# Optimization experiments

Hardware: AMD Instinct MI355X
Metric: run time of the kernel (lower is better)

## Reference

```python
import jax, jax.numpy as jnp
import numpy as np

D_MODEL = 2048
NUM_HEADS = 16
D_K = D_MODEL // NUM_HEADS  # 128, per-head dim used for RoPE
ROPE_THETA = 10000.0
MAX_SEQ_LEN = 2048
BATCH = 4
SEQ = 2048


def _trunc_normal(key, shape, std):
    # approximate trunc_normal_(mean=0, std, a=-3std, b=3std)
    return jnp.clip(std * jax.random.normal(key, shape), -3 * std, 3 * std)


def setup_inputs() -> dict:
    key = jax.random.key(0)
    ks = jax.random.split(key, 6)
    x = jax.random.normal(ks[0], (BATCH, SEQ, D_MODEL), dtype=jnp.float32)
    token_positions = jnp.arange(SEQ, dtype=jnp.int32)
    std = float(np.sqrt(2.0 / (D_MODEL + D_MODEL)))
    wq = _trunc_normal(ks[1], (D_MODEL, D_MODEL), std)  # (d_out, d_in)
    wk = _trunc_normal(ks[2], (D_MODEL, D_MODEL), std)
    wv = _trunc_normal(ks[3], (D_MODEL, D_MODEL), std)
    wo = _trunc_normal(ks[4], (D_MODEL, D_MODEL), std)
    return {"x": x, "token_positions": token_positions,
            "wq": wq, "wk": wk, "wv": wv, "wo": wo}


def _rope(t, pos):
    # t: (b, h, n, d_k), pos: (n,) int
    # interleaved pairs: (x1, x2) = (t[..., 0::2], t[..., 1::2])
    freqs = 1.0 / (ROPE_THETA ** (jnp.arange(0, D_K, 2, dtype=jnp.float32) / D_K))
    angles = pos.astype(jnp.float32)[:, None] * freqs[None, :]  # (n, d_k/2)
    cos = jnp.cos(angles).astype(t.dtype)
    sin = jnp.sin(angles).astype(t.dtype)
    tr = t.reshape(*t.shape[:-1], D_K // 2, 2)
    x1, x2 = tr[..., 0], tr[..., 1]
    y1 = cos * x1 - sin * x2
    y2 = sin * x1 + cos * x2
    return jnp.stack([y1, y2], axis=-1).reshape(t.shape)


def reference(x, token_positions, wq, wk, wv, wo):
    b, n, d = x.shape
    q = jnp.einsum('bnd,od->bno', x, wq)
    k = jnp.einsum('bnd,od->bno', x, wk)
    v = jnp.einsum('bnd,od->bno', x, wv)
    # split heads for RoPE: (b, n, h*dk) -> (b, h, n, dk)
    split = lambda t: t.reshape(b, n, NUM_HEADS, D_K).transpose(0, 2, 1, 3)
    merge = lambda t: t.transpose(0, 2, 1, 3).reshape(b, n, d)
    q = merge(_rope(split(q), token_positions))
    k = merge(_rope(split(k), token_positions))
    # NOTE: source merges heads back BEFORE flash attention -> single-head
    # attention over full d_model with causal mask, scale 1/sqrt(d_model)
    scale = 1.0 / jnp.sqrt(jnp.asarray(d, dtype=x.dtype))
    scores = jnp.einsum('bqd,bkd->bqk', q, k) * scale  # (b, n, n)
    causal = jnp.tril(jnp.ones((n, n), dtype=bool))
    scores = jnp.where(causal[None, :, :], scores, jnp.finfo(scores.dtype).min)
    attn = jax.nn.softmax(scores, axis=-1)
    out = jnp.einsum('bqk,bkd->bqd', attn, v)
    return jnp.einsum('bnd,od->bno', out, wo)
```

## Files before the change

### kernel.cpp

```cpp
#include <hip/hip_runtime.h>
#include <hip/hip_bf16.h>
#include <cstdint>
#include <cmath>

typedef __attribute__((ext_vector_type(4))) float f32x4;
typedef __attribute__((ext_vector_type(8))) short bf16x8;

#define BAR()   __builtin_amdgcn_s_barrier()
#define PRIO1() __builtin_amdgcn_s_setprio(1)
#define PRIO0() __builtin_amdgcn_s_setprio(0)
#define WAITV4() asm volatile("s_waitcnt vmcnt(4)" ::: "memory")
#define WAITV3() asm volatile("s_waitcnt vmcnt(3)" ::: "memory")
#define WAITV0() asm volatile("s_waitcnt vmcnt(0)" ::: "memory")
#define MM(a,b,c) __builtin_amdgcn_mfma_f32_16x16x32_bf16((a),(b),(c),0,0,0)

__device__ __forceinline__ void gl_lds16(const __hip_bfloat16* g, char* l) {
    __builtin_amdgcn_global_load_lds(
        (const __attribute__((address_space(1))) void*)g,
        (__attribute__((address_space(3))) void*)l, 16, 0, 0);
}
__device__ __forceinline__ void store_c(float* C, size_t i, float v) { C[i] = v; }
__device__ __forceinline__ void store_c(__hip_bfloat16* C, size_t i, float v) { C[i] = __float2bfloat16(v); }

#define STAGEA(nb, kt) do{ gl_lds16(Asrc + (kt),                        lds + (nb)         + wb); \
                           gl_lds16(Asrc + (size_t)128 * lda + (kt),    lds + (nb) +  8192 + wb);}while(0)
#define STAGEB(nb, kt) do{ gl_lds16(Bsrc + (kt),                        lds + (nb) + 16384 + wb); \
                           gl_lds16(Bsrc + (size_t)128 * ldb + (kt),    lds + (nb) + 24576 + wb);}while(0)

template<typename CT>
__global__ __launch_bounds__(512, 2)
void gemm256(const __hip_bfloat16* __restrict__ A, const __hip_bfloat16* __restrict__ B,
             CT* __restrict__ C, int K, int lda, int ldb, int ldc, int nbx,
             float alpha, size_t sA, size_t sB, size_t sC)
{
    __shared__ __align__(1024) char lds[98304];

    const int nwg = gridDim.x;
    const int q8 = nwg >> 3, r8 = nwg & 7;
    const int xcd = blockIdx.x & 7, blk = blockIdx.x >> 3;
    const int wg = (xcd < r8 ? xcd * (q8 + 1) : r8 * (q8 + 1) + (xcd - r8) * q8) + blk;
    const int bm0 = (wg / nbx) * 256, bn0 = (wg % nbx) * 256;

    A += sA * blockIdx.y; B += sB * blockIdx.y; C += sC * blockIdx.y;

    const int tid  = threadIdx.x;
    const int lane = tid & 63;
    const int w    = tid >> 6;
    const int wb   = w * 1024;

    const int rb   = (lane & 15) * 64 + (lane >> 4) * 16;
    const int rswz = rb ^ (((rb >> 9) & 1) << 5);
    const int srA  = (w >> 2) * 8;
    const int srB  = (w & 3) * 4;

    const int q0 = tid * 16;
    const int uq = q0 ^ (((q0 >> 9) & 1) << 5);
    const int r0 = ((q0 >> 10) << 4) | ((uq >> 6) & 15);
    const int c0 = (uq & 63) >> 1;
    const __hip_bfloat16* Asrc = A + (size_t)(bm0 + r0) * lda + c0;
    const __hip_bfloat16* Bsrc = B + (size_t)(bn0 + r0) * ldb + c0;

    f32x4 acc[8][4] = {};
    bf16x8 af[4], bf[4];

    const int nt = K >> 5;

    STAGEA(0, 0); STAGEB(0, 0);
    if (nt > 1) { STAGEA(32768, 32); STAGEB(32768, 32); }

    for (int t = 0; t < nt; ++t) {
        if (t + 1 < nt) WAITV4(); else WAITV0();
        BAR();
        const char* dA = lds + (t % 3) * 32768;
        const char* dB = dA + 16384;
        const int  nbo = ((t + 2) % 3) * 32768;
        const bool pf  = (t + 2 < nt);
        const int  kt  = (t + 2) << 5;

#pragma unroll
        for (int i = 0; i < 4; ++i) af[i] = *(const bf16x8*)(dA + ((srA + i) << 10) + rswz);
#pragma unroll
        for (int i = 0; i < 4; ++i) bf[i] = *(const bf16x8*)(dB + ((srB + i) << 10) + rswz);
        if (pf) STAGEA(nbo, kt);
        BAR();
        PRIO1();
#pragma unroll
        for (int mi = 0; mi < 4; ++mi)
#pragma unroll
            for (int ni = 0; ni < 4; ++ni)
                acc[mi][ni] = MM(af[mi], bf[ni], acc[mi][ni]);
        PRIO0();

#pragma unroll
        for (int i = 0; i < 4; ++i) af[i] = *(const bf16x8*)(dA + ((srA + 4 + i) << 10) + rswz);
        if (pf) STAGEB(nbo, kt);
        BAR();
        PRIO1();
#pragma unroll
        for (int mi = 0; mi < 4; ++mi)
#pragma unroll
            for (int ni = 0; ni < 4; ++ni)
                acc[4 + mi][ni] = MM(af[mi], bf[ni], acc[4 + mi][ni]);
        PRIO0();
    }

    const int cr = (lane >> 4) * 4, cc = lane & 15;
    const int wrow = bm0 + (w >> 2) * 128, wcol = bn0 + (w & 3) * 64;
#pragma unroll
    for (int mi = 0; mi < 8; ++mi)
#pragma unroll
        for (int ni = 0; ni < 4; ++ni) {
            const int row = wrow + mi * 16 + cr;
            const int col = wcol + ni * 16 + cc;
#pragma unroll
            for (int j = 0; j < 4; ++j)
                store_c(C, (size_t)(row + j) * ldc + col, acc[mi][ni][j] * alpha);
        }
}

#define STG128(buf, kt) do{ \
    gl_lds16(Asrc + (kt),  lds + (buf) * 24576 +         w * 1024); \
    gl_lds16(Bsrc0 + (kt), lds + (buf) * 24576 +  8192 + w * 1024); \
    gl_lds16(Bsrc1 + (kt), lds + (buf) * 24576 + 16384 + w * 1024); }while(0)

template<typename CT, int MODE>
__global__ __launch_bounds__(512, 4)
void gemm128(const __hip_bfloat16* __restrict__ A, const __hip_bfloat16* __restrict__ B,
             CT* __restrict__ C, int K, int lda, int ldb, int ldc, int nbx,
             float alpha, size_t sA, size_t sB, size_t sC)
{
    __shared__ __align__(1024) char lds[73728];

    int bm0, bn0;
    if (MODE == 1) {
        int g = blockIdx.x, r = 0;
        while (g >= (r >> 1) + 1) { g -= (r >> 1) + 1; ++r; }
        bm0 = r << 7; bn0 = g << 8;
    } else if (MODE == 2) {
        const int g = blockIdx.x;
        const int nby = gridDim.x / nbx;
        const int bx = g % nbx;
        const int by = (g / nbx + bx) % nby;
        bm0 = by << 7; bn0 = bx << 8;
    } else {
        const int nwg = gridDim.x;
        const int q8 = nwg >> 3, r8 = nwg & 7;
        const int xcd = blockIdx.x & 7, blk = blockIdx.x >> 3;
        const int wg = (xcd < r8 ? xcd * (q8 + 1) : r8 * (q8 + 1) + (xcd - r8) * q8) + blk;
        bm0 = (wg / nbx) << 7; bn0 = (wg % nbx) << 8;
    }

    A += sA * blockIdx.y; B += sB * blockIdx.y; C += sC * blockIdx.y;

    const int tid  = threadIdx.x;
    const int lane = tid & 63;
    const int w    = tid >> 6;

    const int rb   = (lane & 15) * 64 + (lane >> 4) * 16;
    const int rswz = rb ^ (((rb >> 9) & 1) << 5);
    const int stA  = (w >> 2) * 4;
    const int stB  = (w & 3) * 4;

    const int qA  = tid * 16;
    const int uqA = qA ^ (((qA >> 9) & 1) << 5);
    const int rA  = ((qA >> 10) << 4) | ((uqA >> 6) & 15);
    const int cA  = (uqA & 63) >> 1;
    const int qB1  = 8192 + tid * 16;
    const int uqB1 = qB1 ^ (((qB1 >> 9) & 1) << 5);
    const int rB1  = ((qB1 >> 10) << 4) | ((uqB1 >> 6) & 15);
    const int cB1  = (uqB1 & 63) >> 1;
    const __hip_bfloat16* Asrc  = A + (size_t)(bm0 + rA) * lda + cA;
    const __hip_bfloat16* Bsrc0 = B + (size_t)(bn0 + rA) * ldb + cA;
    const __hip_bfloat16* Bsrc1 = B + (size_t)(bn0 + rB1) * ldb + cB1;

    f32x4 acc[4][4] = {};
    bf16x8 af[4], bf[4];

    const int klim = bm0 + 128;
    const int kend = (MODE == 2) ? (K < klim ? K : klim) : K;
    const int nt   = kend >> 5;

    STG128(0, 0);
    if (nt > 1) STG128(1, 32);

    for (int t = 0; t < nt; ++t) {
        if (t + 1 < nt) WAITV3(); else WAITV0();
        BAR();
        const char* dA = lds + (t % 3) * 24576;
        const char* dB = dA + 8192;
#pragma unroll
        for (int i = 0; i < 4; ++i) af[i] = *(const bf16x8*)(dA + ((stA + i) << 10) + rswz);
#pragma unroll
        for (int i = 0; i < 4; ++i) bf[i] = *(const bf16x8*)(dB + ((stB + i) << 10) + rswz);
        if (t + 2 < nt) STG128((t + 2) % 3, (t + 2) << 5);
        PRIO1();
#pragma unroll
        for (int mi = 0; mi < 4; ++mi)
#pragma unroll
            for (int ni = 0; ni < 4; ++ni)
                acc[mi][ni] = MM(af[mi], bf[ni], acc[mi][ni]);
        PRIO0();
    }

    const int cr = (lane >> 4) * 4, cc = lane & 15;
    const int wrow = bm0 + (w >> 2) * 64, wcol = bn0 + (w & 3) * 64;
#pragma unroll
    for (int mi = 0; mi < 4; ++mi)
#pragma unroll
        for (int ni = 0; ni < 4; ++ni) {
            const int row = wrow + mi * 16 + cr;
            const int col = wcol + ni * 16 + cc;
#pragma unroll
            for (int j = 0; j < 4; ++j)
                store_c(C, (size_t)(row + j) * ldc + col, acc[mi][ni][j] * alpha);
        }
}

__global__ void f32_to_bf16_vec(const float* __restrict__ in,
                                __hip_bfloat16* __restrict__ out, int n4)
{
    int i = blockIdx.x * 256 + threadIdx.x;
    if (i >= n4) return;
    float4 v = ((const float4*)in)[i];
    union { ushort4 u; __hip_bfloat16 h[4]; } o;
    o.h[0] = __float2bfloat16(v.x);
    o.h[1] = __float2bfloat16(v.y);
    o.h[2] = __float2bfloat16(v.z);
    o.h[3] = __float2bfloat16(v.w);
    ((ushort4*)out)[i] = o.u;
}

__global__ void conv_w4(const float* __restrict__ w0, const float* __restrict__ w1,
                        const float* __restrict__ w2, const float* __restrict__ w3,
                        __hip_bfloat16* o0, __hip_bfloat16* o1,
                        __hip_bfloat16* o2, __hip_bfloat16* o3, int n4)
{
    int i = blockIdx.x * 256 + threadIdx.x;
    if (i >= n4) return;
    const float* src; __hip_bfloat16* dst;
    switch (blockIdx.y) {
        case 0: src = w0; dst = o0; break;
        case 1: src = w1; dst = o1; break;
        case 2: src = w2; dst = o2; break;
        default: src = w3; dst = o3; break;
    }
    float4 v = ((const float4*)src)[i];
    union { ushort4 u; __hip_bfloat16 h[4]; } o;
    o.h[0] = __float2bfloat16(v.x);
    o.h[1] = __float2bfloat16(v.y);
    o.h[2] = __float2bfloat16(v.z);
    o.h[3] = __float2bfloat16(v.w);
    ((ushort4*)dst)[i] = o.u;
}

__global__ void rope_table(const int* __restrict__ pos, float2* __restrict__ tab, int N)
{
    int i = blockIdx.x * 256 + threadIdx.x;
    if (i >= N * 64) return;
    int n = i >> 6, j = i & 63;
    float p = (float)pos[n];
    float ang = p * powf(10000.f, -(float)j * (1.0f / 64.0f));
    tab[i] = make_float2(cosf(ang), sinf(ang));
}

__global__ void rope_apply2(__hip_bfloat16* __restrict__ Q, __hip_bfloat16* __restrict__ K,
                            const float2* __restrict__ tab)
{
    int i = blockIdx.x * 256 + threadIdx.x;
    __hip_bfloat16* T = blockIdx.y ? K : Q;
    int r  = i >> 8;
    int cb = (i & 255) << 3;
    int n  = r & 2047;
    int j0 = (cb >> 1) & 63;
    union { bf16x8 v; __hip_bfloat162 h[4]; } u;
    __hip_bfloat16* p = T + ((size_t)r << 11) + cb;
    u.v = *(const bf16x8*)p;
#pragma unroll
    for (int k = 0; k < 4; ++k) {
        float2 cs = tab[(n << 6) + j0 + k];
        float x1 = __bfloat162float(u.h[k].x);
        float x2 = __bfloat162float(u.h[k].y);
        u.h[k].x = __float2bfloat16(cs.x * x1 - cs.y * x2);
        u.h[k].y = __float2bfloat16(cs.y * x1 + cs.x * x2);
    }
    *(bf16x8*)p = u.v;
}

__global__ void softmax_causal_ip(float* __restrict__ S, int N)
{
    const int q = blockIdx.x;
    float* srow = S + ((size_t)blockIdx.y * N + q) * N;
    __shared__ float buf[2048];
    __shared__ float red[8];
    const int tid = threadIdx.x;

    float4* b4 = (float4*)buf;
    const float4* s4 = (const float4*)srow;
    for (int i = tid; i < N / 4; i += 256) b4[i] = s4[i];
    __syncthreads();

    float m = -1e30f;
    for (int j = tid; j <= q; j += 256) m = fmaxf(m, buf[j]);
#pragma unroll
    for (int o = 32; o > 0; o >>= 1) m = fmaxf(m, __shfl_xor(m, o));
    if ((tid & 63) == 0) red[tid >> 6] = m;
    __syncthreads();
    m = fmaxf(fmaxf(red[0], red[1]), fmaxf(red[2], red[3]));

    float sum = 0.f;
    for (int j = tid; j <= q; j += 256) { float e = __expf(buf[j] - m); buf[j] = e; sum += e; }
#pragma unroll
    for (int o = 32; o > 0; o >>= 1) sum += __shfl_xor(sum, o);
    if ((tid & 63) == 0) red[4 + (tid >> 6)] = sum;
    __syncthreads();
    const float inv = 1.f / (red[4] + red[5] + red[6] + red[7]);

    __hip_bfloat162* p2 = (__hip_bfloat162*)srow;
    for (int i = tid; i < N / 2; i += 256) {
        int j0 = i * 2;
        __hip_bfloat162 h;
        h.x = __float2bfloat16(j0     <= q ? buf[j0]     * inv : 0.f);
        h.y = __float2bfloat16(j0 + 1 <= q ? buf[j0 + 1] * inv : 0.f);
        p2[i] = h;
    }
}

__global__ void transpose_bf16(const __hip_bfloat16* __restrict__ V,
                               __hip_bfloat16* __restrict__ Vt, int N)
{
    __shared__ __hip_bfloat16 tile[32][33];
    const size_t bo = (size_t)blockIdx.z * N * N;
    const int k0 = blockIdx.x * 32, d0 = blockIdx.y * 32;
    const int tx = threadIdx.x, ty = threadIdx.y;
#pragma unroll
    for (int j = 0; j < 4; ++j)
        tile[ty + 8 * j][tx] = V[bo + (size_t)(k0 + ty + 8 * j) * N + d0 + tx];
    __syncthreads();
#pragma unroll
    for (int j = 0; j < 4; ++j)
        Vt[bo + (size_t)(d0 + ty + 8 * j) * N + k0 + tx] = tile[tx][ty + 8 * j];
}

extern "C" void kernel_launch(void* const* d_in, const int* in_sizes, int n_in,
                              void* d_out, int out_size, void* d_ws, size_t ws_size,
                              hipStream_t stream)
{
    const float* x  = (const float*)d_in[0];
    const int* pos  = (const int*)d_in[1];
    const float* wq = (const float*)d_in[2];
    const float* wk = (const float*)d_in[3];
    const float* wv = (const float*)d_in[4];
    const float* wo = (const float*)d_in[5];
    float* out = (float*)d_out;

    const int B = 4, N = 2048, D = 2048;
    const int M = B * N;
    const size_t MB = 1ull << 20;
    if (ws_size < 192 * MB) return;

    char* w = (char*)d_ws;
    __hip_bfloat16* Qb  = (__hip_bfloat16*)(w + 0 * MB);
    __hip_bfloat16* Kb  = (__hip_bfloat16*)(w + 32 * MB);
    __hip_bfloat16* Vb  = (__hip_bfloat16*)(w + 64 * MB);
    __hip_bfloat16* wqb = (__hip_bfloat16*)(w + 96 * MB);
    __hip_bfloat16* wkb = (__hip_bfloat16*)(w + 104 * MB);
    __hip_bfloat16* wvb = (__hip_bfloat16*)(w + 112 * MB);
    __hip_bfloat16* wob = (__hip_bfloat16*)(w + 120 * MB);
    __hip_bfloat16* xb  = (__hip_bfloat16*)(w + 128 * MB);
    __hip_bfloat16* Vt  = xb;
    __hip_bfloat16* AO  = (__hip_bfloat16*)(w + 160 * MB);
    float2*         tab = (float2*)(w + 190 * MB);

    float* Sal = (float*)d_out;

    f32_to_bf16_vec<<<(M * D / 4 + 255) / 256, 256, 0, stream>>>(x, xb, M * D / 4);
    conv_w4<<<dim3((D * D / 4 + 255) / 256, 4), 256, 0, stream>>>(
        wq, wk, wv, wo, wqb, wkb, wvb, wob, D * D / 4);
    rope_table<<<(N * 64 + 255) / 256, 256, 0, stream>>>(pos, tab, N);

    gemm128<__hip_bfloat16, 0><<<dim3((D / 256) * (M / 128)), 512, 0, stream>>>(
        xb, wqb, Qb, D, D, D, D, D / 256, 1.f, 0, 0, 0);
    gemm128<__hip_bfloat16, 0><<<dim3((D / 256) * (M / 128)), 512, 0, stream>>>(
        xb, wkb, Kb, D, D, D, D, D / 256, 1.f, 0, 0, 0);
    gemm256<__hip_bfloat16><<<dim3((D / 256) * (M / 256)), 512, 0, stream>>>(
        xb, wvb, Vb, D, D, D, D, D / 256, 1.f, 0, 0, 0);

    rope_apply2<<<dim3(M * 256 / 256, 2), 256, 0, stream>>>(Qb, Kb, tab);

    transpose_bf16<<<dim3(N / 32, N / 32, B), dim3(32, 8), 0, stream>>>(Vb, Vt, N);

    const float scale = 1.0f / sqrtf((float)D);
    gemm128<float, 1><<<dim3(72, B), 512, 0, stream>>>(
        Qb, Kb, Sal, D, D, D, N, N / 256, scale, (size_t)N * D, (size_t)N * D, (size_t)N * N);
    softmax_causal_ip<<<dim3(N, B), 256, 0, stream>>>(Sal, N);
    gemm128<__hip_bfloat16, 2><<<dim3((N / 128) * (N / 256), B), 512, 0, stream>>>(
        (const __hip_bfloat16*)Sal, Vt, AO, N, 2 * N, D, D, N / 256, 1.f,
        (size_t)2 * N * N, (size_t)N * D, (size_t)N * D);

    gemm256<float><<<dim3((D / 256) * (M / 256)), 512, 0, stream>>>(
        AO, wob, out, D, D, D, D, D / 256, 1.f, 0, 0, 0);
}
```

Measured before the change: 493.8 us.

## Fuse QKV projections into one GEMM and software-pipeline LDS fragment loads

The Q, K and V projection weights are now stored contiguously, so a single 256-tile GEMM writes an interleaved QKV buffer with row stride 3*D in place of three separate GEMM launches. RoPE, the V transpose and the QK^T GEMM are updated to use that stride. Both GEMM kernels are restructured so the next tile's LDS fragments are read while the current MFMAs run, and the global prefetch is issued once per iteration. The aim is to cut launch overhead and tail effects and to hide LDS read latency, at the cost of more fragment registers and strided Q/K/V access in downstream kernels.

```diff
diff --git a/kernel.cpp b/kernel.cpp
--- a/kernel.cpp
+++ b/kernel.cpp
@@ -30,8 +30,7 @@
 template<typename CT>
 __global__ __launch_bounds__(512, 2)
 void gemm256(const __hip_bfloat16* __restrict__ A, const __hip_bfloat16* __restrict__ B,
-             CT* __restrict__ C, int K, int lda, int ldb, int ldc, int nbx,
-             float alpha, size_t sA, size_t sB, size_t sC)
+             CT* __restrict__ C, int K, int lda, int ldb, int ldc, int nbx, float alpha)
 {
     __shared__ __align__(1024) char lds[98304];
 
@@ -40,8 +39,6 @@
     const int xcd = blockIdx.x & 7, blk = blockIdx.x >> 3;
     const int wg = (xcd < r8 ? xcd * (q8 + 1) : r8 * (q8 + 1) + (xcd - r8) * q8) + blk;
     const int bm0 = (wg / nbx) * 256, bn0 = (wg % nbx) * 256;
-
-    A += sA * blockIdx.y; B += sB * blockIdx.y; C += sC * blockIdx.y;
 
     const int tid  = threadIdx.x;
     const int lane = tid & 63;
@@ -61,47 +58,62 @@
     const __hip_bfloat16* Bsrc = B + (size_t)(bn0 + r0) * ldb + c0;
 
     f32x4 acc[8][4] = {};
-    bf16x8 af[4], bf[4];
+    bf16x8 afL[4], afH[4], bfr[4];
 
     const int nt = K >> 5;
 
-    STAGEA(0, 0); STAGEB(0, 0);
-    if (nt > 1) { STAGEA(32768, 32); STAGEB(32768, 32); }
+    STAGEA(0, 0);      STAGEB(0, 0);
+    STAGEA(32768, 32); STAGEB(32768, 32);
+    WAITV4();
+    BAR();
+    {
+        const char* dA = lds; const char* dB = lds + 16384;
+#pragma unroll
+        for (int i = 0; i < 4; ++i) afL[i] = *(const bf16x8*)(dA + ((srA + i) << 10) + rswz);
+#pragma unroll
+        for (int i = 0; i < 4; ++i) bfr[i] = *(const bf16x8*)(dB + ((srB + i) << 10) + rswz);
+    }
 
     for (int t = 0; t < nt; ++t) {
-        if (t + 1 < nt) WAITV4(); else WAITV0();
         BAR();
+        const bool pf = (t + 2) < nt;
+        if (pf) { const int nbo = ((t + 2) % 3) * 32768, kt = (t + 2) << 5;
+                  STAGEA(nbo, kt); STAGEB(nbo, kt); }
+        if (pf) WAITV4(); else WAITV0();
+        BAR();
+
         const char* dA = lds + (t % 3) * 32768;
-        const char* dB = dA + 16384;
-        const int  nbo = ((t + 2) % 3) * 32768;
-        const bool pf  = (t + 2 < nt);
-        const int  kt  = (t + 2) << 5;
-
-#pragma unroll
-        for (int i = 0; i < 4; ++i) af[i] = *(const bf16x8*)(dA + ((srA + i) << 10) + rswz);
-#pragma unroll
-        for (int i = 0; i < 4; ++i) bf[i] = *(const bf16x8*)(dB + ((srB + i) << 10) + rswz);
-        if (pf) STAGEA(nbo, kt);
-        BAR();
+#pragma unroll
+        for (int i = 0; i < 4; ++i) afH[i] = *(const bf16x8*)(dA + ((srA + 4 + i) << 10) + rswz);
+
         PRIO1();
 #pragma unroll
         for (int mi = 0; mi < 4; ++mi)
 #pragma unroll
             for (int ni = 0; ni < 4; ++ni)
-                acc[mi][ni] = MM(af[mi], bf[ni], acc[mi][ni]);
+                acc[mi][ni] = MM(afL[mi], bfr[ni], acc[mi][ni]);
         PRIO0();
 
-#pragma unroll
-        for (int i = 0; i < 4; ++i) af[i] = *(const bf16x8*)(dA + ((srA + 4 + i) << 10) + rswz);
-        if (pf) STAGEB(nbo, kt);
-        BAR();
+        const bool rd = (t + 1) < nt;
+        const char* eA = lds + ((t + 1) % 3) * 32768;
+        if (rd) {
+#pragma unroll
+            for (int i = 0; i < 4; ++i) afL[i] = *(const bf16x8*)(eA + ((srA + i) << 10) + rswz);
+        }
+
         PRIO1();
 #pragma unroll
         for (int mi = 0; mi < 4; ++mi)
 #pragma unroll
             for (int ni = 0; ni < 4; ++ni)
-                acc[4 + mi][ni] = MM(af[mi], bf[ni], acc[4 + mi][ni]);
+                acc[4 + mi][ni] = MM(afH[mi], bfr[ni], acc[4 + mi][ni]);
         PRIO0();
+
+        if (rd) {
+            const char* eB = eA + 16384;
+#pragma unroll
+            for (int i = 0; i < 4; ++i) bfr[i] = *(const bf16x8*)(eB + ((srB + i) << 10) + rswz);
+        }
     }
 
     const int cr = (lane >> 4) * 4, cc = lane & 15;
@@ -136,18 +148,12 @@
         int g = blockIdx.x, r = 0;
         while (g >= (r >> 1) + 1) { g -= (r >> 1) + 1; ++r; }
         bm0 = r << 7; bn0 = g << 8;
-    } else if (MODE == 2) {
+    } else {
         const int g = blockIdx.x;
         const int nby = gridDim.x / nbx;
         const int bx = g % nbx;
         const int by = (g / nbx + bx) % nby;
         bm0 = by << 7; bn0 = bx << 8;
-    } else {
-        const int nwg = gridDim.x;
-        const int q8 = nwg >> 3, r8 = nwg & 7;
-        const int xcd = blockIdx.x & 7, blk = blockIdx.x >> 3;
-        const int wg = (xcd < r8 ? xcd * (q8 + 1) : r8 * (q8 + 1) + (xcd - r8) * q8) + blk;
-        bm0 = (wg / nbx) << 7; bn0 = (wg % nbx) << 8;
     }
 
     A += sA * blockIdx.y; B += sB * blockIdx.y; C += sC * blockIdx.y;
@@ -174,32 +180,59 @@
     const __hip_bfloat16* Bsrc1 = B + (size_t)(bn0 + rB1) * ldb + cB1;
 
     f32x4 acc[4][4] = {};
-    bf16x8 af[4], bf[4];
+    bf16x8 af[4], bfr[4];
 
     const int klim = bm0 + 128;
     const int kend = (MODE == 2) ? (K < klim ? K : klim) : K;
     const int nt   = kend >> 5;
 
-    STG128(0, 0);
-    if (nt > 1) STG128(1, 32);
+    STG128(0, 0); STG128(1, 32);
+    WAITV3();
+    BAR();
+    {
+        const char* dA = lds; const char* dB = lds + 8192;
+#pragma unroll
+        for (int i = 0; i < 4; ++i) af[i]  = *(const bf16x8*)(dA + ((stA + i) << 10) + rswz);
+#pragma unroll
+        for (int i = 0; i < 4; ++i) bfr[i] = *(const bf16x8*)(dB + ((stB + i) << 10) + rswz);
+    }
 
     for (int t = 0; t < nt; ++t) {
-        if (t + 1 < nt) WAITV3(); else WAITV0();
         BAR();
-        const char* dA = lds + (t % 3) * 24576;
-        const char* dB = dA + 8192;
-#pragma unroll
-        for (int i = 0; i < 4; ++i) af[i] = *(const bf16x8*)(dA + ((stA + i) << 10) + rswz);
-#pragma unroll
-        for (int i = 0; i < 4; ++i) bf[i] = *(const bf16x8*)(dB + ((stB + i) << 10) + rswz);
-        if (t + 2 < nt) STG128((t + 2) % 3, (t + 2) << 5);
+        const bool pf = (t + 2) < nt;
+        if (pf) STG128((t + 2) % 3, (t + 2) << 5);
+        if (pf) WAITV3(); else WAITV0();
+        BAR();
+
         PRIO1();
 #pragma unroll
-        for (int mi = 0; mi < 4; ++mi)
-#pragma unroll
-            for (int ni = 0; ni < 4; ++ni)
-                acc[mi][ni] = MM(af[mi], bf[ni], acc[mi][ni]);
+        for (int mi = 0; mi < 4; ++mi) {
+            acc[mi][0] = MM(af[mi], bfr[0], acc[mi][0]);
+            acc[mi][1] = MM(af[mi], bfr[1], acc[mi][1]);
+        }
         PRIO0();
+
+        const bool rd = (t + 1) < nt;
+        const char* eD = lds + ((t + 1) % 3) * 24576;
+        if (rd) {
+            bfr[0] = *(const bf16x8*)(eD + 8192 + ((stB + 0) << 10) + rswz);
+            bfr[1] = *(const bf16x8*)(eD + 8192 + ((stB + 1) << 10) + rswz);
+        }
+
+        PRIO1();
+#pragma unroll
+        for (int mi = 0; mi < 4; ++mi) {
+            acc[mi][2] = MM(af[mi], bfr[2], acc[mi][2]);
+            acc[mi][3] = MM(af[mi], bfr[3], acc[mi][3]);
+        }
+        PRIO0();
+
+        if (rd) {
+#pragma unroll
+            for (int i = 0; i < 4; ++i) af[i] = *(const bf16x8*)(eD + ((stA + i) << 10) + rswz);
+            bfr[2] = *(const bf16x8*)(eD + 8192 + ((stB + 2) << 10) + rswz);
+            bfr[3] = *(const bf16x8*)(eD + 8192 + ((stB + 3) << 10) + rswz);
+        }
     }
 
     const int cr = (lane >> 4) * 4, cc = lane & 15;
@@ -264,7 +297,7 @@
 }
 
 __global__ void rope_apply2(__hip_bfloat16* __restrict__ Q, __hip_bfloat16* __restrict__ K,
-                            const float2* __restrict__ tab)
+                            const float2* __restrict__ tab, int ld)
 {
     int i = blockIdx.x * 256 + threadIdx.x;
     __hip_bfloat16* T = blockIdx.y ? K : Q;
@@ -273,7 +306,7 @@
     int n  = r & 2047;
     int j0 = (cb >> 1) & 63;
     union { bf16x8 v; __hip_bfloat162 h[4]; } u;
-    __hip_bfloat16* p = T + ((size_t)r << 11) + cb;
+    __hip_bfloat16* p = T + (size_t)r * ld + cb;
     u.v = *(const bf16x8*)p;
 #pragma unroll
     for (int k = 0; k < 4; ++k) {
@@ -326,15 +359,16 @@
 }
 
 __global__ void transpose_bf16(const __hip_bfloat16* __restrict__ V,
-                               __hip_bfloat16* __restrict__ Vt, int N)
+                               __hip_bfloat16* __restrict__ Vt, int N, int ldv)
 {
     __shared__ __hip_bfloat16 tile[32][33];
+    const size_t bi = (size_t)blockIdx.z * N * ldv;
     const size_t bo = (size_t)blockIdx.z * N * N;
     const int k0 = blockIdx.x * 32, d0 = blockIdx.y * 32;
     const int tx = threadIdx.x, ty = threadIdx.y;
 #pragma unroll
     for (int j = 0; j < 4; ++j)
-        tile[ty + 8 * j][tx] = V[bo + (size_t)(k0 + ty + 8 * j) * N + d0 + tx];
+        tile[ty + 8 * j][tx] = V[bi + (size_t)(k0 + ty + 8 * j) * ldv + d0 + tx];
     __syncthreads();
 #pragma unroll
     for (int j = 0; j < 4; ++j)
@@ -355,48 +389,46 @@
 
     const int B = 4, N = 2048, D = 2048;
     const int M = B * N;
+    const int D3 = 3 * D;
     const size_t MB = 1ull << 20;
     if (ws_size < 192 * MB) return;
 
     char* w = (char*)d_ws;
-    __hip_bfloat16* Qb  = (__hip_bfloat16*)(w + 0 * MB);
-    __hip_bfloat16* Kb  = (__hip_bfloat16*)(w + 32 * MB);
-    __hip_bfloat16* Vb  = (__hip_bfloat16*)(w + 64 * MB);
-    __hip_bfloat16* wqb = (__hip_bfloat16*)(w + 96 * MB);
-    __hip_bfloat16* wkb = (__hip_bfloat16*)(w + 104 * MB);
-    __hip_bfloat16* wvb = (__hip_bfloat16*)(w + 112 * MB);
-    __hip_bfloat16* wob = (__hip_bfloat16*)(w + 120 * MB);
-    __hip_bfloat16* xb  = (__hip_bfloat16*)(w + 128 * MB);
-    __hip_bfloat16* Vt  = xb;
-    __hip_bfloat16* AO  = (__hip_bfloat16*)(w + 160 * MB);
-    float2*         tab = (float2*)(w + 190 * MB);
+    __hip_bfloat16* QKV  = (__hip_bfloat16*)(w + 0 * MB);
+    __hip_bfloat16* wqkv = (__hip_bfloat16*)(w + 96 * MB);
+    __hip_bfloat16* wob  = (__hip_bfloat16*)(w + 120 * MB);
+    __hip_bfloat16* xb   = (__hip_bfloat16*)(w + 128 * MB);
+    __hip_bfloat16* Vt   = xb;
+    __hip_bfloat16* AO   = (__hip_bfloat16*)(w + 160 * MB);
+    float2*         tab  = (float2*)(w + 190 * MB);
+
+    __hip_bfloat16* Qb = QKV;
+    __hip_bfloat16* Kb = QKV + D;
+    __hip_bfloat16* Vb = QKV + 2 * D;
 
     float* Sal = (float*)d_out;
 
     f32_to_bf16_vec<<<(M * D / 4 + 255) / 256, 256, 0, stream>>>(x, xb, M * D / 4);
     conv_w4<<<dim3((D * D / 4 + 255) / 256, 4), 256, 0, stream>>>(
-        wq, wk, wv, wo, wqb, wkb, wvb, wob, D * D / 4);
+        wq, wk, wv, wo, wqkv, wqkv + (size_t)D * D, wqkv + (size_t)2 * D * D, wob, D * D / 4);
     rope_table<<<(N * 64 + 255) / 256, 256, 0, stream>>>(pos, tab, N);
 
-    gemm128<__hip_bfloat16, 0><<<dim3((D / 256) * (M / 128)), 512, 0, stream>>>(
-        xb, wqb, Qb, D, D, D, D, D / 256, 1.f, 0, 0, 0);
-    gemm128<__hip_bfloat16, 0><<<dim3((D / 256) * (M / 128)), 512, 0, stream>>>(
-        xb, wkb, Kb, D, D, D, D, D / 256, 1.f, 0, 0, 0);
-    gemm256<__hip_bfloat16><<<dim3((D / 256) * (M / 256)), 512, 0, stream>>>(
-        xb, wvb, Vb, D, D, D, D, D / 256, 1.f, 0, 0, 0);
-
-    rope_apply2<<<dim3(M * 256 / 256, 2), 256, 0, stream>>>(Qb, Kb, tab);
-
-    transpose_bf16<<<dim3(N / 32, N / 32, B), dim3(32, 8), 0, stream>>>(Vb, Vt, N);
+    gemm256<__hip_bfloat16><<<dim3((D3 / 256) * (M / 256)), 512, 0, stream>>>(
+        xb, wqkv, QKV, D, D, D, D3, D3 / 256, 1.f);
+
+    rope_apply2<<<dim3(M, 2), 256, 0, stream>>>(Qb, Kb, tab, D3);
+
+    transpose_bf16<<<dim3(N / 32, N / 32, B), dim3(32, 8), 0, stream>>>(Vb, Vt, N, D3);
 
     const float scale = 1.0f / sqrtf((float)D);
     gemm128<float, 1><<<dim3(72, B), 512, 0, stream>>>(
-        Qb, Kb, Sal, D, D, D, N, N / 256, scale, (size_t)N * D, (size_t)N * D, (size_t)N * N);
+        Qb, Kb, Sal, D, D3, D3, N, N / 256, scale,
+        (size_t)N * D3, (size_t)N * D3, (size_t)N * N);
     softmax_causal_ip<<<dim3(N, B), 256, 0, stream>>>(Sal, N);
     gemm128<__hip_bfloat16, 2><<<dim3((N / 128) * (N / 256), B), 512, 0, stream>>>(
-        (const __hip_bfloat16*)Sal, Vt, AO, N, 2 * N, D, D, N / 256, 1.f,
-        (size_t)2 * N * N, (size_t)N * D, (size_t)N * D);
+        (const __hip_bfloat16*)Sal, Vt, AO, N, 2 * N, N, D, N / 256, 1.f,
+        (size_t)2 * N * N, (size_t)N * N, (size_t)N * D);
 
     gemm256<float><<<dim3((D / 256) * (M / 256)), 512, 0, stream>>>(
-        AO, wob, out, D, D, D, D, D / 256, 1.f, 0, 0, 0);
-}
+        AO, wob, out, D, D, D, D, D / 256, 1.f);
+}
```

Measured after the change: 509.2 us. 3.1% more time.
